# Optimization experiments

Hardware: AMD Instinct MI355X
Metric: run time of the kernel (lower is better)

The kernel has to match this reference:

```python
import jax, jax.numpy as jnp
import numpy as np

# config (matches init_kwargs)
NUM_HEADS = 16
HEAD_SIZE = 64
HIDDEN = 1024
NUM_HASHES = 2
NUM_BUCKETS = 128
CHUNK_LEN = 64
N_BEFORE = 1
N_AFTER = 0
IS_DECODER = True
HASH_SEED = 0
MASK_VAL = -1e9      # causal mask value
SELF_MASK_VAL = -1e5  # self-attention mask value
EPS = 1e-6


def setup_inputs() -> dict:
    key = jax.random.key(0)
    k1, k2, k3 = jax.random.split(key, 3)
    hidden_states = jax.random.normal(k1, (2, 4096, HIDDEN), dtype=jnp.float32)
    # nn.Linear weights (out, in), no bias
    Wqk = jax.random.normal(k2, (NUM_HEADS * HEAD_SIZE, HIDDEN), dtype=jnp.float32) * (HIDDEN ** -0.5)
    Wv = jax.random.normal(k3, (NUM_HEADS * HEAD_SIZE, HIDDEN), dtype=jnp.float32) * (HIDDEN ** -0.5)
    # random rotations exactly as the torch module: np.random.seed(hash_seed)
    np.random.seed(HASH_SEED)
    rotations = jnp.asarray(
        np.random.normal(size=(HEAD_SIZE, NUM_HASHES, NUM_BUCKETS // 2)), dtype=jnp.float32)
    return {"hidden_states": hidden_states, "Wqk": Wqk, "Wv": Wv, "rotations": rotations}


def _look_adjacent(x):
    # x: [B, H, n_chunks, chunk, ...]; concat rolled copies along chunk-content axis (3)
    if N_BEFORE == 0 and N_AFTER == 0:
        return x
    slices = [jnp.roll(x, -i, axis=2) for i in range(-N_BEFORE, N_AFTER + 1)]
    return jnp.concatenate(slices, axis=3)


def _lsh_forward(hidden_states, Wqk, Wv, rotations):
    B, S, _ = hidden_states.shape
    H, D, NH = NUM_HEADS, HEAD_SIZE, NUM_HASHES

    # projections -> [B, H, S, D]
    qk = (hidden_states @ Wqk.T).reshape(B, S, H, D).transpose(0, 2, 1, 3)
    v = (hidden_states @ Wv.T).reshape(B, S, H, D).transpose(0, 2, 1, 3)

    # --- hashing ---
    rotated = jnp.einsum('bhsd,dnr->bhnsr', qk, rotations)      # [B,H,NH,S,NB/2]
    rotated = jnp.concatenate([rotated, -rotated], axis=-1)      # [B,H,NH,S,NB]
    buckets = jnp.argmax(rotated, axis=-1)                       # [B,H,NH,S]
    offsets = (jnp.arange(NH) * NUM_BUCKETS)[:, None]            # [NH,1]
    buckets = (buckets + offsets).reshape(B, H, NH * S)          # [B,H,NH*S]

    # --- ticker sort ---
    ticker = jnp.arange(NH * S)
    buckets_and_t = S * buckets + (ticker % S)                   # unique keys
    sorted_ticker = jnp.argsort(buckets_and_t, axis=-1)          # [B,H,NH*S]
    undo_ticker = jnp.argsort(sorted_ticker, axis=-1)
    st = sorted_ticker % S                                       # position indices

    # --- gather (expand over hashes via modded ticker) ---
    qk_s = jnp.take_along_axis(qk, st[..., None], axis=2)        # [B,H,NH*S,D]
    v_s = jnp.take_along_axis(v, st[..., None], axis=2)

    n_chunks = (NH * S) // CHUNK_LEN
    qk_c = qk_s.reshape(B, H, n_chunks, CHUNK_LEN, D)
    v_c = v_s.reshape(B, H, n_chunks, CHUNK_LEN, D)
    tick_c = st.reshape(B, H, n_chunks, CHUNK_LEN)

    # key = len-and-dim norm of query_key
    var = jnp.mean(qk_c * qk_c, axis=-1, keepdims=True)
    key_c = qk_c * jax.lax.rsqrt(var + EPS) / jnp.sqrt(jnp.asarray(D, qk_c.dtype))

    kk = _look_adjacent(key_c)                                   # [B,H,n_chunks,K,D], K=(1+before+after)*chunk
    vv = _look_adjacent(v_c)
    kt = _look_adjacent(tick_c)                                  # [B,H,n_chunks,K]

    dots = jnp.einsum('bhnqd,bhnkd->bhnqk', qk_c, kk)            # [B,H,n_chunks,chunk,K]
    if IS_DECODER:
        causal = tick_c[..., :, None] >= kt[..., None, :]
        dots = jnp.where(causal, dots, MASK_VAL)
    not_self = tick_c[..., :, None] != kt[..., None, :]
    dots = jnp.where(not_self, dots, SELF_MASK_VAL)

    logits = jax.nn.logsumexp(dots, axis=-1, keepdims=True)      # [B,H,n_chunks,chunk,1]
    probs = jnp.exp(dots - logits)
    out = jnp.einsum('bhnqk,bhnkd->bhnqd', probs, vv)            # [B,H,n_chunks,chunk,D]

    out = out.reshape(B, H, NH * S, D)
    logits = logits.reshape(B, H, NH * S)

    # undo sort
    out = jnp.take_along_axis(out, undo_ticker[..., None], axis=2)
    logits = jnp.take_along_axis(logits, undo_ticker, axis=2)

    # combine hash rounds with logsumexp weights
    if NH > 1:
        out = out.reshape(B, H, NH, S, D)
        lg = logits.reshape(B, H, NH, S, 1)
        w = jnp.exp(lg - jax.nn.logsumexp(lg, axis=2, keepdims=True))
        out = jnp.sum(out * w, axis=2)                           # [B,H,S,D]

    # [B,S,H*D]
    return out.transpose(0, 2, 1, 3).reshape(B, S, H * D)


def reference(hidden_states, Wqk, Wv, rotations):
    return _lsh_forward(hidden_states, Wqk, Wv, rotations)
```

## Files before the change

### kernel.cpp

```cpp
#include <hip/hip_runtime.h>


typedef __attribute__((ext_vector_type(4))) float          f32x4;
typedef __attribute__((ext_vector_type(4))) unsigned short u16x4;
typedef __attribute__((ext_vector_type(8))) unsigned short u16x8;
typedef __attribute__((ext_vector_type(8))) __bf16         bf16x8;

__device__ __forceinline__ float bf2f(unsigned short u) {
    unsigned int x = ((unsigned int)u) << 16;
    return __builtin_bit_cast(float, x);
}
__device__ __forceinline__ unsigned short f2bf(float f) {
    unsigned int x = __builtin_bit_cast(unsigned int, f);
    x += 0x7FFFu + ((x >> 16) & 1u);
    return (unsigned short)(x >> 16);
}

__device__ __forceinline__ void gll16(const unsigned short* g, unsigned short* l) {
    __builtin_amdgcn_global_load_lds(
        (__attribute__((address_space(1))) void*)(g),
        (__attribute__((address_space(3))) void*)(l),
        16, 0, 0);
}

__global__ __launch_bounds__(256)
void split_kernel(const float* __restrict__ hidden,
                  const float* __restrict__ wv,
                  unsigned short* __restrict__ hH, unsigned short* __restrict__ hL,
                  unsigned short* __restrict__ wH, unsigned short* __restrict__ wL)
{
    const int idx = blockIdx.x * 256 + threadIdx.x;
    const bool isw = idx >= 2097152;
    const float* src = isw ? wv : hidden;
    unsigned short* dh = isw ? wH : hH;
    unsigned short* dl = isw ? wL : hL;
    const int v = isw ? (idx - 2097152) : idx;
    const f32x4 x = *((const f32x4*)src + v);
    u16x4 h, l;
#pragma unroll
    for (int j = 0; j < 4; ++j) {
        const unsigned short hs = f2bf(x[j]);
        h[j] = hs;
        l[j] = f2bf(x[j] - bf2f(hs));
    }
    *((u16x4*)dh + v) = h;
    *((u16x4*)dl + v) = l;
}

__global__ __launch_bounds__(256)
void gemm_qk(const float* __restrict__ hidden,
             const float* __restrict__ wqk,
             float* __restrict__ qk_out)
{
    __shared__ float As[16][132];
    __shared__ float Bs[16][132];
    const int tid = threadIdx.x;
    const int bm  = blockIdx.x;
    const int bn  = blockIdx.y;

    const float* Asrc = hidden + (size_t)bm * 128 * 1024;
    const float* Bsrc = wqk + (size_t)bn * 128 * 1024;

    const int mlo = (tid & 15) * 4;
    const int nlo = (tid >> 4) * 4;

    float acc[8][8];
#pragma unroll
    for (int r = 0; r < 8; ++r)
#pragma unroll
        for (int c = 0; c < 8; ++c) acc[r][c] = 0.f;

    int srow[2], skof[2];
#pragma unroll
    for (int i = 0; i < 2; ++i) {
        const int c = i * 256 + tid;
        srow[i] = c >> 2;
        skof[i] = (c & 3) * 4;
    }

    f32x4 apre[2], bpre[2];
#pragma unroll
    for (int i = 0; i < 2; ++i) {
        apre[i] = *(const f32x4*)(Asrc + (size_t)srow[i] * 1024 + skof[i]);
        bpre[i] = *(const f32x4*)(Bsrc + (size_t)srow[i] * 1024 + skof[i]);
    }

    for (int ks = 0; ks < 64; ++ks) {
#pragma unroll
        for (int i = 0; i < 2; ++i)
#pragma unroll
            for (int j = 0; j < 4; ++j) {
                As[skof[i] + j][srow[i]] = apre[i][j];
                Bs[skof[i] + j][srow[i]] = bpre[i][j];
            }
        __syncthreads();
        if (ks < 63) {
            const int k0 = (ks + 1) * 16;
#pragma unroll
            for (int i = 0; i < 2; ++i) {
                apre[i] = *(const f32x4*)(Asrc + (size_t)srow[i] * 1024 + k0 + skof[i]);
                bpre[i] = *(const f32x4*)(Bsrc + (size_t)srow[i] * 1024 + k0 + skof[i]);
            }
        }
#pragma unroll
        for (int k = 0; k < 16; ++k) {
            f32x4 a0 = *(const f32x4*)&As[k][mlo];
            f32x4 a1 = *(const f32x4*)&As[k][64 + mlo];
            f32x4 b0 = *(const f32x4*)&Bs[k][nlo];
            f32x4 b1 = *(const f32x4*)&Bs[k][64 + nlo];
#pragma unroll
            for (int c = 0; c < 4; ++c) {
#pragma unroll
                for (int r = 0; r < 4; ++r) {
                    acc[r][c]         = __builtin_fmaf(a0[r], b0[c], acc[r][c]);
                    acc[r][c + 4]     = __builtin_fmaf(a0[r], b1[c], acc[r][c + 4]);
                    acc[r + 4][c]     = __builtin_fmaf(a1[r], b0[c], acc[r + 4][c]);
                    acc[r + 4][c + 4] = __builtin_fmaf(a1[r], b1[c], acc[r + 4][c + 4]);
                }
            }
        }
        __syncthreads();
    }

#pragma unroll
    for (int r = 0; r < 8; ++r) {
        const int mm = (r < 4) ? (mlo + r) : (64 + mlo + (r - 4));
        const int m  = bm * 128 + mm;
        const int bb = m >> 12, s = m & 4095;
#pragma unroll
        for (int g = 0; g < 2; ++g) {
            const int n  = bn * 128 + (g ? (64 + nlo) : nlo);
            const int hh = n >> 6, d = n & 63;
            f32x4 v;
#pragma unroll
            for (int c = 0; c < 4; ++c) v[c] = acc[r][g * 4 + c];
            *(f32x4*)&qk_out[(((size_t)(bb * 16 + hh)) * 4096 + s) * 64 + d] = v;
        }
    }
}

__global__ __launch_bounds__(256)
void gemm_v(const unsigned short* __restrict__ hH,
            const unsigned short* __restrict__ hL,
            const unsigned short* __restrict__ wH,
            const unsigned short* __restrict__ wL,
            unsigned short* __restrict__ v_out)
{
    __shared__ __attribute__((aligned(16))) unsigned short Ah[128 * 32];
    __shared__ __attribute__((aligned(16))) unsigned short Al[128 * 32];
    __shared__ __attribute__((aligned(16))) unsigned short Bh[128 * 32];
    __shared__ __attribute__((aligned(16))) unsigned short Bl[128 * 32];

    const int tid  = threadIdx.x;
    const int bm   = blockIdx.x;
    const int bn   = blockIdx.y;
    const int w    = tid >> 6;
    const int lane = tid & 63;
    const int l16  = lane & 15;
    const int quad = lane >> 4;
    const int m0   = (w >> 1) * 64;
    const int n0   = (w & 1) * 64;

    const int c0 = w * 2;
    const int r0 = c0 * 16 + (lane >> 2);
    const int r1 = r0 + 16;
    const int kf = (lane & 3) * 8;

    const size_t abase = (size_t)bm * 128 * 1024;
    const size_t bbase = (size_t)bn * 128 * 1024;

    f32x4 acc[4][4];
#pragma unroll
    for (int i = 0; i < 4; ++i)
#pragma unroll
        for (int j = 0; j < 4; ++j) acc[i][j] = f32x4{0.f, 0.f, 0.f, 0.f};

    for (int ks = 0; ks < 32; ++ks) {
        const int kb = ks * 32 + kf;
        gll16(hH + abase + (size_t)r0 * 1024 + kb, Ah + (size_t)c0 * 512);
        gll16(hH + abase + (size_t)r1 * 1024 + kb, Ah + (size_t)(c0 + 1) * 512);
        gll16(hL + abase + (size_t)r0 * 1024 + kb, Al + (size_t)c0 * 512);
        gll16(hL + abase + (size_t)r1 * 1024 + kb, Al + (size_t)(c0 + 1) * 512);
        gll16(wH + bbase + (size_t)r0 * 1024 + kb, Bh + (size_t)c0 * 512);
        gll16(wH + bbase + (size_t)r1 * 1024 + kb, Bh + (size_t)(c0 + 1) * 512);
        gll16(wL + bbase + (size_t)r0 * 1024 + kb, Bl + (size_t)c0 * 512);
        gll16(wL + bbase + (size_t)r1 * 1024 + kb, Bl + (size_t)(c0 + 1) * 512);
        __syncthreads();

        bf16x8 ahf[4], alf[4], bhf[4], blf[4];
#pragma unroll
        for (int i = 0; i < 4; ++i) {
            ahf[i] = *(const bf16x8*)&Ah[(m0 + i * 16 + l16) * 32 + quad * 8];
            alf[i] = *(const bf16x8*)&Al[(m0 + i * 16 + l16) * 32 + quad * 8];
        }
#pragma unroll
        for (int j = 0; j < 4; ++j) {
            bhf[j] = *(const bf16x8*)&Bh[(n0 + j * 16 + l16) * 32 + quad * 8];
            blf[j] = *(const bf16x8*)&Bl[(n0 + j * 16 + l16) * 32 + quad * 8];
        }
#pragma unroll
        for (int i = 0; i < 4; ++i)
#pragma unroll
            for (int j = 0; j < 4; ++j) {
                acc[i][j] = __builtin_amdgcn_mfma_f32_16x16x32_bf16(ahf[i], bhf[j], acc[i][j], 0, 0, 0);
                acc[i][j] = __builtin_amdgcn_mfma_f32_16x16x32_bf16(alf[i], bhf[j], acc[i][j], 0, 0, 0);
                acc[i][j] = __builtin_amdgcn_mfma_f32_16x16x32_bf16(ahf[i], blf[j], acc[i][j], 0, 0, 0);
            }
        __syncthreads();
    }

#pragma unroll
    for (int i = 0; i < 4; ++i) {
#pragma unroll
        for (int r = 0; r < 4; ++r) {
            const int m  = bm * 128 + m0 + i * 16 + quad * 4 + r;
            const int bb = m >> 12, s = m & 4095;
#pragma unroll
            for (int j = 0; j < 4; ++j) {
                const int n  = bn * 128 + n0 + j * 16 + l16;
                const int hh = n >> 6, d = n & 63;
                v_out[(((size_t)(bb * 16 + hh)) * 4096 + s) * 64 + d] = f2bf(acc[i][j][r]);
            }
        }
    }
}

__global__ __launch_bounds__(256)
void hash_kernel(const float* __restrict__ qk,
                 const float* __restrict__ rotf,
                 int* __restrict__ buckets)
{
    __shared__ float rot[8192];
    __shared__ float rows[64 * 64];
    const int tid = threadIdx.x;
    for (int i = tid; i < 8192; i += 256) rot[i] = rotf[i];
    const int rbase = blockIdx.x * 64;
    {
        const f32x4* src = (const f32x4*)(qk + (size_t)rbase * 64);
        f32x4* dst = (f32x4*)rows;
#pragma unroll
        for (int i = 0; i < 4; ++i) dst[tid + i * 256] = src[tid + i * 256];
    }
    __syncthreads();
    const int w = tid >> 6, lane = tid & 63;
    for (int rr = 0; rr < 16; ++rr) {
        const int row = w * 16 + rr;
        float a0 = 0.f, a1 = 0.f;
#pragma unroll
        for (int dg = 0; dg < 16; ++dg) {
            f32x4 qb = *(const f32x4*)&rows[row * 64 + dg * 4];
#pragma unroll
            for (int j = 0; j < 4; ++j) {
                const int d = dg * 4 + j;
                a0 = __builtin_fmaf(qb[j], rot[d * 128 + lane],      a0);
                a1 = __builtin_fmaf(qb[j], rot[d * 128 + 64 + lane], a1);
            }
        }
        float v0, v1; int i0, i1;
        if (a0 >= -a0) { v0 = a0;  i0 = lane; } else { v0 = -a0; i0 = 64 + lane; }
        if (a1 >= -a1) { v1 = a1;  i1 = lane; } else { v1 = -a1; i1 = 64 + lane; }
#pragma unroll
        for (int m = 1; m < 64; m <<= 1) {
            float ov = __shfl_xor(v0, m); int oi = __shfl_xor(i0, m);
            if (ov > v0 || (ov == v0 && oi < i0)) { v0 = ov; i0 = oi; }
            ov = __shfl_xor(v1, m); oi = __shfl_xor(i1, m);
            if (ov > v1 || (ov == v1 && oi < i1)) { v1 = ov; i1 = oi; }
        }
        if (lane == 0) {
            const int g = rbase + row;
            const int bh = g >> 12, s = g & 4095;
            buckets[(size_t)bh * 8192 + s]        = i0;
            buckets[(size_t)bh * 8192 + 4096 + s] = i1 + 128;
        }
    }
}

__global__ __launch_bounds__(256)
void sort_kernel(const int* __restrict__ buckets, int* __restrict__ sorted)
{
    __shared__ unsigned char  lb[8192];
    __shared__ unsigned short sl[8192];
    __shared__ int cnt[256];
    __shared__ int base[256];
    __shared__ unsigned short whist[4][256];
    const int tid  = threadIdx.x;
    const int bh   = blockIdx.x;
    const int lane = tid & 63;
    const int w    = tid >> 6;

    cnt[tid] = 0;
    for (int i = tid; i < 8192; i += 256)
        lb[i] = (unsigned char)buckets[(size_t)bh * 8192 + i];
    __syncthreads();
    for (int i = tid; i < 8192; i += 256) atomicAdd(&cnt[lb[i]], 1);
    __syncthreads();

    base[tid] = cnt[tid];
    __syncthreads();
#pragma unroll
    for (int off = 1; off < 256; off <<= 1) {
        int t = (tid >= off) ? base[tid - off] : 0;
        __syncthreads();
        base[tid] += t;
        __syncthreads();
    }
    {
        int ex = base[tid] - cnt[tid];
        __syncthreads();
        base[tid] = ex;
        __syncthreads();
    }

    for (int c = 0; c < 32; ++c) {
        const int i = c * 256 + tid;
        const int b = lb[i];
        whist[0][tid] = 0; whist[1][tid] = 0; whist[2][tid] = 0; whist[3][tid] = 0;
        __syncthreads();
        unsigned long long m = ~0ull;
#pragma unroll
        for (int bit = 0; bit < 8; ++bit) {
            const unsigned long long bb = __ballot((b >> bit) & 1);
            m &= ((b >> bit) & 1) ? bb : ~bb;
        }
        const unsigned long long ltmask = (lane == 63) ? ~0ull >> 1
                                         : ((1ull << lane) - 1);
        const int rank_in_wave = __popcll(m & ltmask);
        if (rank_in_wave == 0)
            whist[w][b] = (unsigned short)__popcll(m);
        __syncthreads();
        int rank = rank_in_wave;
#pragma unroll
        for (int ww = 0; ww < 3; ++ww)
            if (ww < w) rank += whist[ww][b];
        const int pos = base[b] + rank;
        sl[pos] = (unsigned short)i;
        __syncthreads();
        base[tid] += whist[0][tid] + whist[1][tid] + whist[2][tid] + whist[3][tid];
        __syncthreads();
    }

    for (int i = tid; i < 8192; i += 256)
        sorted[(size_t)bh * 8192 + i] = (int)sl[i];
}

#define KQP 72
#define VPP 136

__global__ __launch_bounds__(256)
void attn_kernel(const float* __restrict__ qk,
                 const unsigned short* __restrict__ vb,
                 const int* __restrict__ sorted,
                 unsigned short* __restrict__ out_hash,
                 float* __restrict__ logits)
{
    __shared__ unsigned short kq[128 * KQP];
    __shared__ unsigned short vvt[64 * VPP];
    __shared__ unsigned short Pm[64 * VPP];
    __shared__ float scl[128];
    __shared__ unsigned short stick[128];
    __shared__ unsigned short qtick_lo[64];
    __shared__ unsigned short qtick_hi[64];
    __shared__ float lg[64];
    float* ssqf = (float*)Pm;

    const int tid = threadIdx.x;
    const int c  = blockIdx.x;
    const int bh = blockIdx.z * 16 + blockIdx.y;
    const int pc = (c + 127) & 127;

    if (tid < 128) {
        const int p  = (tid < 64) ? (pc * 64 + tid) : (c * 64 + (tid - 64));
        const int tk = sorted[(size_t)bh * 8192 + p];
        stick[tid] = (unsigned short)(tk & 4095);
        if (tid >= 64) {
            qtick_lo[tid - 64] = (unsigned short)(tk & 4095);
            qtick_hi[tid - 64] = (unsigned short)(tk >> 12);
        }
    }
    __syncthreads();

    {
        const int r = tid >> 1, half = tid & 1;
        const int srow = stick[r];
        const f32x4* src = (const f32x4*)(qk + (((size_t)bh * 4096 + srow) << 6) + half * 32);
        float ss = 0.f;
#pragma unroll
        for (int i = 0; i < 8; ++i) {
            f32x4 x = src[i];
            ss += x[0]*x[0] + x[1]*x[1] + x[2]*x[2] + x[3]*x[3];
            u16x4 uu;
            uu[0] = f2bf(x[0]); uu[1] = f2bf(x[1]);
            uu[2] = f2bf(x[2]); uu[3] = f2bf(x[3]);
            *(u16x4*)&kq[r * KQP + half * 32 + i * 4] = uu;
        }
        ssqf[r * 2 + half] = ss;

        const unsigned short* vs = vb + (((size_t)bh * 4096 + srow) << 6) + half * 32;
        unsigned short vtmp[32];
#pragma unroll
        for (int i = 0; i < 4; ++i)
            *(u16x8*)&vtmp[i * 8] = *(const u16x8*)(vs + i * 8);
#pragma unroll
        for (int j = 0; j < 32; ++j)
            vvt[(half * 32 + j) * VPP + r] = vtmp[j];
    }
    __syncthreads();
    if (tid < 128) {
        const float ss = ssqf[tid * 2] + ssqf[tid * 2 + 1];
        scl[tid] = (1.0f / sqrtf(ss * (1.0f / 64.0f) + 1e-6f)) * 0.125f;
    }
    __syncthreads();

    const int w    = tid >> 6;
    const int lane = tid & 63;
    const int l16  = lane & 15;
    const int quad = lane >> 4;

    f32x4 accS[8];
#pragma unroll
    for (int t = 0; t < 8; ++t) accS[t] = f32x4{0.f, 0.f, 0.f, 0.f};
#pragma unroll
    for (int kst = 0; kst < 2; ++kst) {
        const bf16x8 aq = *(const bf16x8*)&kq[(64 + w * 16 + l16) * KQP + kst * 32 + quad * 8];
#pragma unroll
        for (int t = 0; t < 8; ++t) {
            const bf16x8 bk = *(const bf16x8*)&kq[(t * 16 + l16) * KQP + kst * 32 + quad * 8];
            accS[t] = __builtin_amdgcn_mfma_f32_16x16x32_bf16(aq, bk, accS[t], 0, 0, 0);
        }
    }

    float sct[8]; int tkt[8];
#pragma unroll
    for (int t = 0; t < 8; ++t) {
        sct[t] = scl[t * 16 + l16];
        tkt[t] = (int)stick[t * 16 + l16];
    }
    int tqr[4];
#pragma unroll
    for (int r = 0; r < 4; ++r) tqr[r] = (int)stick[64 + w * 16 + quad * 4 + r];

    float val[8][4];
#pragma unroll
    for (int t = 0; t < 8; ++t)
#pragma unroll
        for (int r = 0; r < 4; ++r) {
            float a = accS[t][r] * sct[t];
            if (tqr[r] <  tkt[t]) a = -1e9f;
            if (tqr[r] == tkt[t]) a = -1e5f;
            val[t][r] = a;
        }

    float inv_r[4], logit_r[4];
#pragma unroll
    for (int r = 0; r < 4; ++r) {
        float m = val[0][r];
#pragma unroll
        for (int t = 1; t < 8; ++t) m = fmaxf(m, val[t][r]);
        m = fmaxf(m, __shfl_xor(m, 1));
        m = fmaxf(m, __shfl_xor(m, 2));
        m = fmaxf(m, __shfl_xor(m, 4));
        m = fmaxf(m, __shfl_xor(m, 8));
        float l = 0.f;
#pragma unroll
        for (int t = 0; t < 8; ++t) { val[t][r] = expf(val[t][r] - m); l += val[t][r]; }
        l += __shfl_xor(l, 1);
        l += __shfl_xor(l, 2);
        l += __shfl_xor(l, 4);
        l += __shfl_xor(l, 8);
        logit_r[r] = m + logf(l);
        inv_r[r]   = 1.0f / l;
    }

#pragma unroll
    for (int t = 0; t < 8; ++t)
#pragma unroll
        for (int r = 0; r < 4; ++r)
            Pm[(w * 16 + quad * 4 + r) * VPP + t * 16 + l16] = f2bf(val[t][r] * inv_r[r]);
    if (l16 == 0) {
#pragma unroll
        for (int r = 0; r < 4; ++r) lg[w * 16 + quad * 4 + r] = logit_r[r];
    }
    __syncthreads();

    f32x4 accO[4];
#pragma unroll
    for (int dt = 0; dt < 4; ++dt) accO[dt] = f32x4{0.f, 0.f, 0.f, 0.f};
#pragma unroll
    for (int kst = 0; kst < 4; ++kst) {
        const bf16x8 ap = *(const bf16x8*)&Pm[(w * 16 + l16) * VPP + kst * 32 + quad * 8];
#pragma unroll
        for (int dt = 0; dt < 4; ++dt) {
            const bf16x8 bv = *(const bf16x8*)&vvt[(dt * 16 + l16) * VPP + kst * 32 + quad * 8];
            accO[dt] = __builtin_amdgcn_mfma_f32_16x16x32_bf16(ap, bv, accO[dt], 0, 0, 0);
        }
    }

    unsigned short* outb = kq;
#pragma unroll
    for (int dt = 0; dt < 4; ++dt)
#pragma unroll
        for (int r = 0; r < 4; ++r)
            outb[(w * 16 + quad * 4 + r) * KQP + dt * 16 + l16] = f2bf(accO[dt][r]);
    __syncthreads();

    if (tid < 64) {
        const int n = qtick_hi[tid], s = qtick_lo[tid];
        logits[((size_t)bh * 2 + n) * 4096 + s] = lg[tid];
    }
    {
        const int qq = tid >> 2, part = tid & 3;
        const int n = qtick_hi[qq], s = qtick_lo[qq];
        const size_t ob = (((size_t)bh * 2 + n) * 4096 + s) * 64 + part * 16;
        u16x8 u0 = *(const u16x8*)&outb[qq * KQP + part * 16];
        u16x8 u1 = *(const u16x8*)&outb[qq * KQP + part * 16 + 8];
        *(u16x8*)(out_hash + ob)     = u0;
        *(u16x8*)(out_hash + ob + 8) = u1;
    }
}

__global__ __launch_bounds__(256)
void combine_kernel(const unsigned short* __restrict__ out_hash,
                    const float* __restrict__ logits,
                    float* __restrict__ out)
{
    const int idx  = blockIdx.x * 256 + threadIdx.x;
    const int bh   = idx >> 16;
    const int rem  = idx & 65535;
    const int s    = rem >> 4;
    const int part = rem & 15;
    const float lg0 = logits[((size_t)bh * 2 + 0) * 4096 + s];
    const float lg1 = logits[((size_t)bh * 2 + 1) * 4096 + s];
    const float m  = fmaxf(lg0, lg1);
    const float e0 = expf(lg0 - m), e1 = expf(lg1 - m);
    const float inv = 1.0f / (e0 + e1);
    const float w0 = e0 * inv, w1 = e1 * inv;
    const size_t b0 = (((size_t)bh * 2 + 0) * 4096 + s) * 64 + part * 4;
    const size_t b1 = (((size_t)bh * 2 + 1) * 4096 + s) * 64 + part * 4;
    u16x4 u0 = *(const u16x4*)(out_hash + b0);
    u16x4 u1 = *(const u16x4*)(out_hash + b1);
    const int b = bh >> 4, hh = bh & 15;
    const size_t ob = ((size_t)b * 4096 + s) * 1024 + hh * 64 + part * 4;
    f32x4 r;
#pragma unroll
    for (int e = 0; e < 4; ++e)
        r[e] = w0 * bf2f(u0[e]) + w1 * bf2f(u1[e]);
    *(f32x4*)(out + ob) = r;
}

extern "C" void kernel_launch(void* const* d_in, const int* in_sizes, int n_in,
                              void* d_out, int out_size, void* d_ws, size_t ws_size,
                              hipStream_t stream) {
    const float* hidden = (const float*)d_in[0];
    const float* wqk    = (const float*)d_in[1];
    const float* wv     = (const float*)d_in[2];
    const float* rotf   = (const float*)d_in[3];
    float* out = (float*)d_out;

    char* ws = (char*)d_ws;
    float*          qk       = (float*)(ws);
    unsigned short* vb       = (unsigned short*)(ws + 33554432);
    int*            buckets  = (int*)(ws + 50331648);
    int*            sorted   = (int*)(ws + 51380224);
    float*          logits   = (float*)(ws + 52428800);
    unsigned short* out_hash = (unsigned short*)(ws + 53477376);
    unsigned short* hH = out_hash;
    unsigned short* hL = out_hash + 8388608;
    unsigned short* wH = (unsigned short*)(ws + 87031808);
    unsigned short* wL = (unsigned short*)(ws + 89128960);

    hipLaunchKernelGGL(split_kernel, dim3(9216),   dim3(256), 0, stream,
                       hidden, wv, hH, hL, wH, wL);
    hipLaunchKernelGGL(gemm_qk,     dim3(64, 8),   dim3(256), 0, stream,
                       hidden, wqk, qk);
    hipLaunchKernelGGL(gemm_v,      dim3(64, 8),   dim3(256), 0, stream,
                       hH, hL, wH, wL, vb);
    hipLaunchKernelGGL(hash_kernel, dim3(2048),    dim3(256), 0, stream,
                       qk, rotf, buckets);
    hipLaunchKernelGGL(sort_kernel, dim3(32),      dim3(256), 0, stream,
                       buckets, sorted);
    hipLaunchKernelGGL(attn_kernel, dim3(128, 16, 2), dim3(256), 0, stream,
                       qk, vb, sorted, out_hash, logits);
    hipLaunchKernelGGL(combine_kernel, dim3(8192), dim3(256), 0, stream,
                       out_hash, logits, out);
}
```

Before: 521.3 us.

## Load B operand straight from global into registers and double-buffer A tile in LDS

The fp32 QK projection GEMM no longer stages the weight tile in shared memory. Each thread instead reads its own B rows directly from global memory into registers, prefetching one 4-wide k-group ahead. The A tile is double-buffered in LDS so only one barrier per k-step is needed, which removes LDS traffic and a sync for B. The cost is more register pressure and uncoalesced, redundant global reads of B: threads with the same nlo read the same rows, leaning on L1/L2.

Measured after the change: 616.4 us. 1.18x slower.

```diff
diff --git a/kernel.cpp b/kernel.cpp
--- a/kernel.cpp
+++ b/kernel.cpp
@@ -52,8 +52,7 @@
              const float* __restrict__ wqk,
              float* __restrict__ qk_out)
 {
-    __shared__ float As[16][132];
-    __shared__ float Bs[16][132];
+    __shared__ float As[2][16][132];
     const int tid = threadIdx.x;
     const int bm  = blockIdx.x;
     const int bn  = blockIdx.y;
@@ -63,6 +62,9 @@
 
     const int mlo = (tid & 15) * 4;
     const int nlo = (tid >> 4) * 4;
+
+    const float* brow0 = Bsrc + (size_t)nlo * 1024;
+    const float* brow1 = Bsrc + (size_t)(64 + nlo) * 1024;
 
     float acc[8][8];
 #pragma unroll
@@ -78,46 +80,64 @@
         skof[i] = (c & 3) * 4;
     }
 
-    f32x4 apre[2], bpre[2];
-#pragma unroll
-    for (int i = 0; i < 2; ++i) {
+    f32x4 apre[2];
+#pragma unroll
+    for (int i = 0; i < 2; ++i)
         apre[i] = *(const f32x4*)(Asrc + (size_t)srow[i] * 1024 + skof[i]);
-        bpre[i] = *(const f32x4*)(Bsrc + (size_t)srow[i] * 1024 + skof[i]);
-    }
+#pragma unroll
+    for (int i = 0; i < 2; ++i)
+#pragma unroll
+        for (int j = 0; j < 4; ++j)
+            As[0][skof[i] + j][srow[i]] = apre[i][j];
+
+    f32x4 b0[2][4], b1[2][4];
+#pragma unroll
+    for (int cc = 0; cc < 4; ++cc) {
+        b0[0][cc] = *(const f32x4*)(brow0 + (size_t)cc * 1024);
+        b1[0][cc] = *(const f32x4*)(brow1 + (size_t)cc * 1024);
+    }
+    __syncthreads();
 
     for (int ks = 0; ks < 64; ++ks) {
-#pragma unroll
-        for (int i = 0; i < 2; ++i)
-#pragma unroll
-            for (int j = 0; j < 4; ++j) {
-                As[skof[i] + j][srow[i]] = apre[i][j];
-                Bs[skof[i] + j][srow[i]] = bpre[i][j];
-            }
-        __syncthreads();
+        const int buf = ks & 1;
         if (ks < 63) {
             const int k0 = (ks + 1) * 16;
 #pragma unroll
-            for (int i = 0; i < 2; ++i) {
+            for (int i = 0; i < 2; ++i)
                 apre[i] = *(const f32x4*)(Asrc + (size_t)srow[i] * 1024 + k0 + skof[i]);
-                bpre[i] = *(const f32x4*)(Bsrc + (size_t)srow[i] * 1024 + k0 + skof[i]);
+        }
+#pragma unroll
+        for (int kg = 0; kg < 4; ++kg) {
+            const int cur = kg & 1, nxt = cur ^ 1;
+            const int nk = (ks * 16 + kg * 4 + 4) & 1023;
+#pragma unroll
+            for (int cc = 0; cc < 4; ++cc) {
+                b0[nxt][cc] = *(const f32x4*)(brow0 + (size_t)cc * 1024 + nk);
+                b1[nxt][cc] = *(const f32x4*)(brow1 + (size_t)cc * 1024 + nk);
             }
-        }
-#pragma unroll
-        for (int k = 0; k < 16; ++k) {
-            f32x4 a0 = *(const f32x4*)&As[k][mlo];
-            f32x4 a1 = *(const f32x4*)&As[k][64 + mlo];
-            f32x4 b0 = *(const f32x4*)&Bs[k][nlo];
-            f32x4 b1 = *(const f32x4*)&Bs[k][64 + nlo];
-#pragma unroll
-            for (int c = 0; c < 4; ++c) {
-#pragma unroll
-                for (int r = 0; r < 4; ++r) {
-                    acc[r][c]         = __builtin_fmaf(a0[r], b0[c], acc[r][c]);
-                    acc[r][c + 4]     = __builtin_fmaf(a0[r], b1[c], acc[r][c + 4]);
-                    acc[r + 4][c]     = __builtin_fmaf(a1[r], b0[c], acc[r + 4][c]);
-                    acc[r + 4][c + 4] = __builtin_fmaf(a1[r], b1[c], acc[r + 4][c + 4]);
+#pragma unroll
+            for (int j = 0; j < 4; ++j) {
+                const int k = kg * 4 + j;
+                f32x4 a0 = *(const f32x4*)&As[buf][k][mlo];
+                f32x4 a1 = *(const f32x4*)&As[buf][k][64 + mlo];
+#pragma unroll
+                for (int c = 0; c < 4; ++c) {
+#pragma unroll
+                    for (int r = 0; r < 4; ++r) {
+                        acc[r][c]         = __builtin_fmaf(a0[r], b0[cur][c][j], acc[r][c]);
+                        acc[r][c + 4]     = __builtin_fmaf(a0[r], b1[cur][c][j], acc[r][c + 4]);
+                        acc[r + 4][c]     = __builtin_fmaf(a1[r], b0[cur][c][j], acc[r + 4][c]);
+                        acc[r + 4][c + 4] = __builtin_fmaf(a1[r], b1[cur][c][j], acc[r + 4][c + 4]);
+                    }
                 }
             }
+        }
+        if (ks < 63) {
+#pragma unroll
+            for (int i = 0; i < 2; ++i)
+#pragma unroll
+                for (int j = 0; j < 4; ++j)
+                    As[buf ^ 1][skof[i] + j][srow[i]] = apre[i][j];
         }
         __syncthreads();
     }
```
